# Performance work log

Measured on AMD Instinct MI355X. Metric: run time of the kernel, lower is better.

The kernel has to match this reference:

```python
import jax, jax.numpy as jnp
import numpy as np

PRECS = 1e-6
# [min, max] scaling ranges for the 12 XAJ parameters (order matches parameters[:, i, :])
PARA_SCALE = [[0.3, 2.0], [0.0, 5.0], [0.01, 100.0], [0.01, 100.0], [0.01, 200.0],
              [0.09, 1.0], [0.01, 100.0], [0.0, 10.0], [0.01, 0.7], [0.01, 0.7],
              [0.0, 0.998], [0.0, 0.998]]


def setup_inputs() -> dict:
    key = jax.random.key(0)
    k1, k2 = jax.random.split(key)
    Nstep, Ngrid, mu = 365, 2000, 8
    # col 0 = P (mm/d), col 2 = PET (mm/d); col 1 unused by the model
    x = jax.random.uniform(k1, (Nstep, Ngrid, 3), dtype=jnp.float32) * 10.0
    parameters = jax.random.uniform(k2, (Ngrid, 12, mu), dtype=jnp.float32)
    return {"x": x, "parameters": parameters, "mu": mu}


def _xaj(x, parameters, mu):
    P = x[:, :, 0]          # [T, Ngrid]
    PET = x[:, :, 2]        # [T, Ngrid]  (index 2, matching the original code)
    Ngrid = x.shape[1]

    sc = lambda a, i: PARA_SCALE[i][0] + a * (PARA_SCALE[i][1] - PARA_SCALE[i][0])
    (parKE, parB, parWUM, parWLM, parWM, parC, parSM, parEX,
     parKI_, parKG_, parCI, parCG) = [sc(parameters[:, i, :], i) for i in range(12)]

    wdm = jnp.maximum(parWM - parWUM - parWLM, 0.0)
    sum_k = parKI_ + parKG_
    parKI = jnp.where(sum_k < 1.0, parKI_, (1.0 - PRECS) * parKI_ / (sum_k + PRECS))
    parKG = jnp.where(sum_k < 1.0, parKG_, (1.0 - PRECS) * parKG_ / (sum_k + PRECS))

    init_state = jnp.full((Ngrid, mu), 0.001, dtype=jnp.float32)
    WU0 = WL0 = WD0 = S0 = QI0 = QG0 = FR0_init = init_state

    def step(carry, inp):
        WU, WL, WD, S, FR0, QI, QG = carry
        P_row, PET_row = inp                      # each [Ngrid]
        P_t = P_row[:, None]                      # broadcast over mu
        PET_t = PET_row[:, None] * parKE

        # three-layer evapotranspiration
        EU = jnp.minimum(PET_t, WU + P_t)
        D = jnp.maximum(PET_t - EU, 0.0)
        wet_excess = jnp.maximum(WL - parC * parWLM, 0.0)
        wet_ratio = wet_excess / (wet_excess + 1.0)
        EL_wet = D * WL / (parWLM + PRECS)
        EL_dry = jnp.minimum(parC * D, WL)
        EL = jnp.maximum(wet_ratio * EL_wet + (1.0 - wet_ratio) * EL_dry, 0.0)
        EL = jnp.minimum(EL, WL)
        D_res = jnp.maximum(D - EL, 0.0)
        ED = jnp.minimum(parC * D_res, WD)
        E = EU + EL + ED

        # saturation-excess runoff
        PE = jnp.maximum(P_t - E, 0.0)
        W = WU + WL + WD
        WMM = parWM * (1.0 + parB)
        base_W = jnp.maximum(1.0 - W / (parWM + PRECS), PRECS)
        A = WMM * (1.0 - base_W ** (1.0 / (1.0 + parB)))
        ratio = jnp.minimum((PE + A) / (WMM + PRECS), 1.0)
        R_per = jnp.where(PE + A < WMM,
                          PE - (parWM - W) + parWM * (1.0 - ratio) ** (1.0 + parB),
                          PE - (parWM - W))
        R_per = jnp.maximum(R_per, 0.0)

        # soil moisture update (fill top-down, deplete top-down)
        dW = P_t - E - R_per
        dpos = jnp.maximum(dW, 0.0)
        fill_u = jnp.minimum(dpos, jnp.maximum(parWUM - WU, 0.0))
        WU = WU + fill_u; dpos = dpos - fill_u
        fill_l = jnp.minimum(dpos, jnp.maximum(parWLM - WL, 0.0))
        WL = WL + fill_l; dpos = dpos - fill_l
        fill_d = jnp.minimum(dpos, jnp.maximum(wdm - WD, 0.0))
        WD = WD + fill_d
        dneg = jnp.maximum(-dW, 0.0)
        sub_u = jnp.minimum(dneg, WU)
        WU = WU - sub_u; dneg = dneg - sub_u
        sub_l = jnp.minimum(dneg, WL)
        WL = WL - sub_l; dneg = dneg - sub_l
        sub_d = jnp.minimum(dneg, WD)
        WD = WD - sub_d

        # free-water reservoir + three-flow separation
        FR_new = R_per / (PE + PRECS)
        FR = jnp.where(PE > 0.0, FR_new, FR0)
        FR = jnp.clip(FR, 0.0, 1.0)
        S_eq = jnp.minimum(S * FR0 / (FR + PRECS), parSM)
        SMM = parSM * (1.0 + parEX)
        ratio_s = jnp.maximum(1.0 - S_eq / (parSM + PRECS), PRECS)
        AU = SMM * (1.0 - ratio_s ** (1.0 / (1.0 + parEX)))
        ratio_pa = jnp.minimum((PE + AU) / (SMM + PRECS), 1.0)
        RS1 = (PE + S_eq - parSM + parSM * (1.0 - ratio_pa) ** (1.0 + parEX)) * FR
        RS2 = (PE + S_eq - parSM) * FR
        RS = jnp.where(PE + AU < SMM, RS1, RS2)
        RS = jnp.minimum(jnp.maximum(RS, 0.0), R_per)
        S = jnp.minimum(S_eq + (R_per - RS) / (FR + PRECS), parSM)
        RI = parKI * S * FR
        RG = parKG * S * FR
        S = S * (1.0 - parKI - parKG)

        # linear reservoirs
        QI = parCI * QI + (1.0 - parCI) * RI
        QG = parCG * QG + (1.0 - parCG) * RG

        return (WU, WL, WD, S, FR, QI, QG), (RS, QI, QG, E)

    carry0 = (WU0, WL0, WD0, S0, FR0_init, QI0, QG0)
    _, (QS_inflow, QI_inflow, QG_inflow, ET_series) = jax.lax.scan(step, carry0, (P, PET))

    QSave = QS_inflow.mean(-1, keepdims=True)
    QIave = QI_inflow.mean(-1, keepdims=True)
    QGave = QG_inflow.mean(-1, keepdims=True)
    ETave = ET_series.mean(-1, keepdims=True)
    river_inflow = QS_inflow + QI_inflow + QG_inflow
    Qs = river_inflow.mean(-1, keepdims=True)   # muwts is None
    # [Nstep, Ngrid, 5]
    return jnp.concatenate([Qs, QSave, QIave, QGave, ETave], axis=-1)


def reference(x, parameters, mu):
    return _xaj(x, parameters, mu)
```

## Files before the change

kernel.cpp:

```cpp
#include <hip/hip_runtime.h>

#define PRECS 1e-6f

__device__ __forceinline__ float fpow(float b, float e) {
    return __builtin_amdgcn_exp2f(e * __builtin_amdgcn_logf(b));
}

__device__ __forceinline__ float frcp(float v) {
    return __builtin_amdgcn_rcpf(v);
}

__device__ __forceinline__ float med3(float a, float b, float c) {
    return __builtin_amdgcn_fmed3f(a, b, c);
}

template <int CTRL>
__device__ __forceinline__ float dpp_mov(float v) {
    return __int_as_float(
        __builtin_amdgcn_update_dpp(0, __float_as_int(v), CTRL, 0xF, 0xF, true));
}

__device__ __forceinline__ float rsum8(float v) {
    v += dpp_mov<0xB1>(v);
    v += dpp_mov<0x4E>(v);
    v += dpp_mov<0x141>(v);
    return v;
}

__global__ __launch_bounds__(256, 1) void xaj_kernel(
    const float* __restrict__ x,
    const float* __restrict__ prm,
    float* __restrict__ out)
{
    constexpr int Nstep = 365, Ngrid = 2000;
    constexpr int xstride = Ngrid * 3;
    constexpr int K = 16;
    constexpr int NBLK = 23;
    constexpr int NPH  = NBLK + 3;

    const int wid  = (int)threadIdx.x >> 6;
    const int lane = (int)threadIdx.x & 63;
    const int g = blockIdx.x * 8 + (lane >> 3);
    const int m = lane & 7;

    __shared__ float2 stIn[2][K][64];
    __shared__ float4 stA[4][K][64];
    __shared__ float4 stFR[2][K][64];
    __shared__ float4 stB[2][K][64];

    const float lo[12] = {0.3f,0.0f,0.01f,0.01f,0.01f,0.09f,0.01f,0.0f,0.01f,0.01f,0.0f,0.0f};
    const float hi[12] = {2.0f,5.0f,100.0f,100.0f,200.0f,1.0f,100.0f,10.0f,0.7f,0.7f,0.998f,0.998f};
    float p[12];
    const float* pb = prm + (size_t)g * 96 + m;
#pragma unroll
    for (int i = 0; i < 12; ++i)
        p[i] = lo[i] + pb[i * 8] * (hi[i] - lo[i]);

    const float KE=p[0], B=p[1], WUM=p[2], WLM=p[3], WM=p[4], C=p[5],
                SM=p[6], EX=p[7], KI_=p[8], KG_=p[9], CI=p[10], CG=p[11];

    const float wdm  = fmaxf(WM - WUM - WLM, 0.f);
    const float sumk = KI_ + KG_;
    const float nrm  = (1.f - PRECS) / (sumk + PRECS);
    const float KI   = (sumk < 1.f) ? KI_ : KI_ * nrm;
    const float KG   = (sumk < 1.f) ? KG_ : KG_ * nrm;
    const float expB = 1.f + B,  invB  = 1.f / expB;
    const float WMM  = WM * expB;
    const float expEX= 1.f + EX, invEX = 1.f / expEX;
    const float SMM  = SM * expEX;
    const float inv_WLM = 1.f / (WLM + PRECS);
    const float inv_WM  = 1.f / (WM  + PRECS);
    const float inv_WMM = 1.f / (WMM + PRECS);
    const float inv_SM  = 1.f / (SM  + PRECS);
    const float inv_SMM = 1.f / (SMM + PRECS);
    const float oneK = 1.f - KI - KG;
    const float omCI = 1.f - CI, omCG = 1.f - CG;
    const float CWLM = C * WLM;
    const float inv1p = 1.f / (1.f + PRECS);
    const float eps2  = fmaxf(PRECS, fmaf(-SM, inv_SM, 1.f));
    const float powPRECS = fpow(PRECS, invB);

    float WU = 0.001f, WL = 0.001f, WD = 0.001f;
    float pw1;
    {
        const float W0 = 0.003f;
        pw1 = fpow(fmaxf(fmaf(-W0, inv_WM, 1.f), PRECS), invB);
    }
    float weC0   = fmaxf(WL - CWLM, 0.f);
    float wrC    = weC0 * frcp(1.f + weC0);
    float wlinvC = WL * inv_WLM;

    float Snc = 0.001f / oneK;
    float FRc = 0.001f, iFRc = frcp(0.001f + PRECS);
    float QI = 0.001f, QG = 0.001f;
    const float cKI = omCI * KI, cKG = omCG * KG;
    const float wa = (m == 0 || m == 1) ? 0.125f : 0.f;
    const float wb = (m == 0 || m == 2) ? 0.125f : 0.f;
    const float wc = (m == 0 || m == 3) ? 0.125f : 0.f;
    const float wd = (m >= 4) ? 0.125f : 0.f;
    const int   col = (m < 4) ? m : 4;
    float* outp = out + (size_t)g * 5 + col;
    const size_t ostr = (size_t)Ngrid * 5;
    const float* xg = x + (size_t)g * 3;
    float Pr[K], Er[K];

    auto ASTEP = [&](int ibuf, int obuf) {
        float2 rin[K];
#pragma unroll
        for (int k = 0; k < K; ++k)
            rin[k] = stIn[ibuf][k][lane];
#pragma unroll
        for (int k = 0; k < K; ++k) {
            const float Pt = rin[k].x, PET_t = rin[k].y;
            const float PETmP = PET_t - Pt;
            const float capD  = fmaxf(wdm, WD);
            const float M0 = fminf(PETmP, WU);
            const float D  = fmaxf(PETmP - WU, 0.f);
            const float ELwet = D * wlinvC;
            const float CD    = C * D;
            const float ELdry = fminf(CD, WL);
            const float EL    = med3(fmaf(wrC, ELwet - ELdry, ELdry), 0.f, WL);
            const float ED    = med3(fmaf(-C, EL, CD), 0.f, WD);
            const float SUME  = (M0 + EL) + ED;
            const float PE    = fmaxf(-SUME, 0.f);
            const float E     = Pt + SUME;
            const float W     = (WU + WL) + WD;
            const float omr   = fmaxf(fmaf(-PE, inv_WMM, pw1), 0.f);
            const float powr  = fpow(omr, expB);
            const float R_per = fmaxf(fmaf(WM, powr, PE + (W - WM)), 0.f);
            const float bwd  = fmaxf(fmaf(-(W - SUME), inv_WM, 1.f), PRECS);
            const float pw1d = fpow(bwd, invB);
            pw1 = (SUME < 0.f) ? fmaxf(omr, powPRECS) : pw1d;
            const float c0  = (WU - SUME) - R_per;
            const float WUn = med3(c0, 0.f, WUM);
            const float c1  = WL + (c0 - WUn);
            const float WLn = med3(c1, 0.f, WLM);
            const float c2  = WD + (c1 - WLn);
            const float WDn = med3(c2, 0.f, capD);
            WU = WUn; WL = WLn; WD = WDn;
            const float weN = fmaxf(WLn - CWLM, 0.f);
            wrC    = weN * frcp(1.f + weN);
            wlinvC = WLn * inv_WLM;
            stA[obuf][k][lane] = make_float4(PE, R_per, E, 0.f);
        }
    };

    auto BSTEP = [&](int abuf, int fbuf) {
        float4 ra[K], rg[K];
#pragma unroll
        for (int k = 0; k < K; ++k) ra[k] = stA[abuf][k][lane];
#pragma unroll
        for (int k = 0; k < K; ++k) rg[k] = stFR[fbuf][k][lane];
#pragma unroll
        for (int k = 0; k < K; ++k) {
            const float PE = ra[k].x, R_per = ra[k].y;
            const float FR = rg[k].x, iFR = rg[k].y;
            const float giFR = rg[k].z, r2 = rg[k].w;
            const float RpiFR = R_per * iFR;
            const float corr  = RpiFR - PE;
            const float S_eq    = fminf(Snc * giFR, SM);
            const float ratio_s = fmaxf(fmaf(-Snc, r2, 1.f), eps2);
            const float u   = fpow(ratio_s, invEX);
            const float om2 = fmaxf(fmaf(-PE, inv_SMM, u), 0.f);
            const float q   = fpow(om2, expEX);
            const float T   = fmaf(-SM, q, SM - S_eq);
            const float mq  = med3(T + corr, 0.f, RpiFR);
            const float Sn  = S_eq + mq;
            const float base = (PE - SM) + S_eq;
            const float RS = med3(fmaf(SM, q, base) * FR, 0.f, R_per);
            stB[fbuf][k][lane] = make_float4(RS, FR * Sn, ra[k].z, 0.f);
            Snc = Sn;
        }
    };

    auto CISSUE = [&](int blk) {
#pragma unroll
        for (int k = 0; k < K; ++k) {
            int t = blk * K + k;
            t = (t < Nstep) ? t : Nstep - 1;
            const float* xq = xg + (size_t)t * xstride;
            Pr[k] = xq[0];
            Er[k] = xq[2];
        }
    };
    auto CFR = [&](int abuf, int fbuf) {
#pragma unroll
        for (int k = 0; k < K; ++k) {
            const float4 ra = stA[abuf][k][lane];
            const float gk = oneK * FRc;
            const float q  = frcp(ra.x + PRECS);
            const float aa = ra.y * q;
            const float FRn  = fminf(aa, 1.f);
            const float iFRn = fmaxf(frcp(aa + PRECS), inv1p);
            const bool wet = ra.x > 0.f;
            FRc  = wet ? FRn  : FRc;
            iFRc = wet ? iFRn : iFRc;
            const float giFR = gk * iFRc;
            const float r2   = giFR * inv_SM;
            stFR[fbuf][k][lane] = make_float4(FRc, iFRc, giFR, r2);
        }
    };
    auto CWRITE = [&](int buf) {
#pragma unroll
        for (int k = 0; k < K; ++k)
            stIn[buf][k][lane] = make_float2(Pr[k], Er[k] * KE);
    };

    auto DSTEP = [&](int bbuf, int blk) {
        float4 rb[K];
#pragma unroll
        for (int k = 0; k < K; ++k) rb[k] = stB[bbuf][k][lane];
        const int t0 = blk * K;
#pragma unroll
        for (int k = 0; k < K; ++k) {
            QI = fmaf(CI, QI, cKI * rb[k].y);
            QG = fmaf(CG, QG, cKG * rb[k].y);
            const float u0 = rsum8(rb[k].x);
            const float u1 = rsum8(QI);
            const float u2 = rsum8(QG);
            const float u3 = rsum8(rb[k].z);
            const float v = fmaf(u0, wa, fmaf(u1, wb, fmaf(u2, wc, u3 * wd)));
            if (t0 + k < Nstep)
                outp[(size_t)(t0 + k) * ostr] = v;
        }
    };

    if (wid == 2) { CISSUE(0); CWRITE(0); }
    __syncthreads();

#pragma unroll 1
    for (int ph = 0; ph < NPH; ++ph) {
        if (wid == 0) {
            if (ph < NBLK) ASTEP(ph & 1, ph & 3);
        } else if (wid == 1) {
            if (ph >= 2 && ph < NBLK + 2) BSTEP((ph - 2) & 3, (ph - 2) & 1);
        } else if (wid == 2) {
            const bool ld = (ph + 1 < NBLK);
            if (ld) CISSUE(ph + 1);
            if (ph >= 1 && ph < NBLK + 1)
                CFR((ph - 1) & 3, (ph - 1) & 1);
            if (ld) CWRITE((ph + 1) & 1);
        } else {
            if (ph >= 3) DSTEP((ph - 3) & 1, ph - 3);
        }
        __syncthreads();
    }
}

extern "C" void kernel_launch(void* const* d_in, const int* in_sizes, int n_in,
                              void* d_out, int out_size, void* d_ws, size_t ws_size,
                              hipStream_t stream) {
    const float* x   = (const float*)d_in[0];
    const float* prm = (const float*)d_in[1];
    float* out = (float*)d_out;
    xaj_kernel<<<250, 256, 0, stream>>>(x, prm, out);
}
```

Before: 57.75 us.

## Replace lockstep block barriers with LDS flag-based producer-consumer pipeline between waves

The four specialized waves no longer advance in lockstep phases separated by __syncthreads. Each wave now runs its own loop and waits on per-stage LDS counters (acquire/release atomics with s_sleep polling). Input staging is deepened to four buffers so loads run two blocks ahead. Some work is also shifted: the A stage precomputes PE*inv_SMM, the FR stage precomputes R_per*iFR, the B stage uses a simplified med3 clamp for S, and stB shrinks to float2, with E read directly from stA. The aim is to let faster waves run ahead and remove barrier stalls, at the cost of spin-wait overhead and more complex buffer-reuse ordering.

After: 61.14 us. 1.06x slower.

```diff
diff --git a/kernel.cpp b/kernel.cpp
--- a/kernel.cpp
+++ b/kernel.cpp
@@ -25,6 +25,15 @@
     v += dpp_mov<0x4E>(v);
     v += dpp_mov<0x141>(v);
     return v;
+}
+
+__device__ __forceinline__ void waitge(int* f, int v) {
+    while (__hip_atomic_load(f, __ATOMIC_ACQUIRE, __HIP_MEMORY_SCOPE_WORKGROUP) < v)
+        __builtin_amdgcn_s_sleep(1);
+}
+__device__ __forceinline__ void setflag(int* f, int v) {
+    if ((threadIdx.x & 63) == 0)
+        __hip_atomic_store(f, v, __ATOMIC_RELEASE, __HIP_MEMORY_SCOPE_WORKGROUP);
 }
 
 __global__ __launch_bounds__(256, 1) void xaj_kernel(
@@ -36,17 +45,17 @@
     constexpr int xstride = Ngrid * 3;
     constexpr int K = 16;
     constexpr int NBLK = 23;
-    constexpr int NPH  = NBLK + 3;
 
     const int wid  = (int)threadIdx.x >> 6;
     const int lane = (int)threadIdx.x & 63;
     const int g = blockIdx.x * 8 + (lane >> 3);
     const int m = lane & 7;
 
-    __shared__ float2 stIn[2][K][64];
+    __shared__ float2 stIn[4][K][64];
     __shared__ float4 stA[4][K][64];
     __shared__ float4 stFR[2][K][64];
-    __shared__ float4 stB[2][K][64];
+    __shared__ float2 stB[2][K][64];
+    __shared__ int flg[8];
 
     const float lo[12] = {0.3f,0.0f,0.01f,0.01f,0.01f,0.09f,0.01f,0.0f,0.01f,0.01f,0.0f,0.0f};
     const float hi[12] = {2.0f,5.0f,100.0f,100.0f,200.0f,1.0f,100.0f,10.0f,0.7f,0.7f,0.998f,0.998f};
@@ -80,170 +89,184 @@
     const float eps2  = fmaxf(PRECS, fmaf(-SM, inv_SM, 1.f));
     const float powPRECS = fpow(PRECS, invB);
 
-    float WU = 0.001f, WL = 0.001f, WD = 0.001f;
-    float pw1;
-    {
-        const float W0 = 0.003f;
-        pw1 = fpow(fmaxf(fmaf(-W0, inv_WM, 1.f), PRECS), invB);
-    }
-    float weC0   = fmaxf(WL - CWLM, 0.f);
-    float wrC    = weC0 * frcp(1.f + weC0);
-    float wlinvC = WL * inv_WLM;
-
-    float Snc = 0.001f / oneK;
-    float FRc = 0.001f, iFRc = frcp(0.001f + PRECS);
-    float QI = 0.001f, QG = 0.001f;
-    const float cKI = omCI * KI, cKG = omCG * KG;
-    const float wa = (m == 0 || m == 1) ? 0.125f : 0.f;
-    const float wb = (m == 0 || m == 2) ? 0.125f : 0.f;
-    const float wc = (m == 0 || m == 3) ? 0.125f : 0.f;
-    const float wd = (m >= 4) ? 0.125f : 0.f;
-    const int   col = (m < 4) ? m : 4;
-    float* outp = out + (size_t)g * 5 + col;
-    const size_t ostr = (size_t)Ngrid * 5;
     const float* xg = x + (size_t)g * 3;
-    float Pr[K], Er[K];
-
-    auto ASTEP = [&](int ibuf, int obuf) {
-        float2 rin[K];
-#pragma unroll
-        for (int k = 0; k < K; ++k)
-            rin[k] = stIn[ibuf][k][lane];
-#pragma unroll
-        for (int k = 0; k < K; ++k) {
-            const float Pt = rin[k].x, PET_t = rin[k].y;
-            const float PETmP = PET_t - Pt;
-            const float capD  = fmaxf(wdm, WD);
-            const float M0 = fminf(PETmP, WU);
-            const float D  = fmaxf(PETmP - WU, 0.f);
-            const float ELwet = D * wlinvC;
-            const float CD    = C * D;
-            const float ELdry = fminf(CD, WL);
-            const float EL    = med3(fmaf(wrC, ELwet - ELdry, ELdry), 0.f, WL);
-            const float ED    = med3(fmaf(-C, EL, CD), 0.f, WD);
-            const float SUME  = (M0 + EL) + ED;
-            const float PE    = fmaxf(-SUME, 0.f);
-            const float E     = Pt + SUME;
-            const float W     = (WU + WL) + WD;
-            const float omr   = fmaxf(fmaf(-PE, inv_WMM, pw1), 0.f);
-            const float powr  = fpow(omr, expB);
-            const float R_per = fmaxf(fmaf(WM, powr, PE + (W - WM)), 0.f);
-            const float bwd  = fmaxf(fmaf(-(W - SUME), inv_WM, 1.f), PRECS);
-            const float pw1d = fpow(bwd, invB);
-            pw1 = (SUME < 0.f) ? fmaxf(omr, powPRECS) : pw1d;
-            const float c0  = (WU - SUME) - R_per;
-            const float WUn = med3(c0, 0.f, WUM);
-            const float c1  = WL + (c0 - WUn);
-            const float WLn = med3(c1, 0.f, WLM);
-            const float c2  = WD + (c1 - WLn);
-            const float WDn = med3(c2, 0.f, capD);
-            WU = WUn; WL = WLn; WD = WDn;
-            const float weN = fmaxf(WLn - CWLM, 0.f);
-            wrC    = weN * frcp(1.f + weN);
-            wlinvC = WLn * inv_WLM;
-            stA[obuf][k][lane] = make_float4(PE, R_per, E, 0.f);
-        }
-    };
-
-    auto BSTEP = [&](int abuf, int fbuf) {
-        float4 ra[K], rg[K];
-#pragma unroll
-        for (int k = 0; k < K; ++k) ra[k] = stA[abuf][k][lane];
-#pragma unroll
-        for (int k = 0; k < K; ++k) rg[k] = stFR[fbuf][k][lane];
-#pragma unroll
-        for (int k = 0; k < K; ++k) {
-            const float PE = ra[k].x, R_per = ra[k].y;
-            const float FR = rg[k].x, iFR = rg[k].y;
-            const float giFR = rg[k].z, r2 = rg[k].w;
-            const float RpiFR = R_per * iFR;
-            const float corr  = RpiFR - PE;
-            const float S_eq    = fminf(Snc * giFR, SM);
-            const float ratio_s = fmaxf(fmaf(-Snc, r2, 1.f), eps2);
-            const float u   = fpow(ratio_s, invEX);
-            const float om2 = fmaxf(fmaf(-PE, inv_SMM, u), 0.f);
-            const float q   = fpow(om2, expEX);
-            const float T   = fmaf(-SM, q, SM - S_eq);
-            const float mq  = med3(T + corr, 0.f, RpiFR);
-            const float Sn  = S_eq + mq;
-            const float base = (PE - SM) + S_eq;
-            const float RS = med3(fmaf(SM, q, base) * FR, 0.f, R_per);
-            stB[fbuf][k][lane] = make_float4(RS, FR * Sn, ra[k].z, 0.f);
-            Snc = Sn;
-        }
-    };
-
-    auto CISSUE = [&](int blk) {
-#pragma unroll
-        for (int k = 0; k < K; ++k) {
-            int t = blk * K + k;
-            t = (t < Nstep) ? t : Nstep - 1;
-            const float* xq = xg + (size_t)t * xstride;
-            Pr[k] = xq[0];
-            Er[k] = xq[2];
-        }
-    };
-    auto CFR = [&](int abuf, int fbuf) {
-#pragma unroll
-        for (int k = 0; k < K; ++k) {
-            const float4 ra = stA[abuf][k][lane];
-            const float gk = oneK * FRc;
-            const float q  = frcp(ra.x + PRECS);
-            const float aa = ra.y * q;
-            const float FRn  = fminf(aa, 1.f);
-            const float iFRn = fmaxf(frcp(aa + PRECS), inv1p);
-            const bool wet = ra.x > 0.f;
-            FRc  = wet ? FRn  : FRc;
-            iFRc = wet ? iFRn : iFRc;
-            const float giFR = gk * iFRc;
-            const float r2   = giFR * inv_SM;
-            stFR[fbuf][k][lane] = make_float4(FRc, iFRc, giFR, r2);
-        }
-    };
-    auto CWRITE = [&](int buf) {
-#pragma unroll
-        for (int k = 0; k < K; ++k)
-            stIn[buf][k][lane] = make_float2(Pr[k], Er[k] * KE);
-    };
-
-    auto DSTEP = [&](int bbuf, int blk) {
-        float4 rb[K];
-#pragma unroll
-        for (int k = 0; k < K; ++k) rb[k] = stB[bbuf][k][lane];
-        const int t0 = blk * K;
-#pragma unroll
-        for (int k = 0; k < K; ++k) {
-            QI = fmaf(CI, QI, cKI * rb[k].y);
-            QG = fmaf(CG, QG, cKG * rb[k].y);
-            const float u0 = rsum8(rb[k].x);
-            const float u1 = rsum8(QI);
-            const float u2 = rsum8(QG);
-            const float u3 = rsum8(rb[k].z);
-            const float v = fmaf(u0, wa, fmaf(u1, wb, fmaf(u2, wc, u3 * wd)));
-            if (t0 + k < Nstep)
-                outp[(size_t)(t0 + k) * ostr] = v;
-        }
-    };
-
-    if (wid == 2) { CISSUE(0); CWRITE(0); }
+
+    if (threadIdx.x < 8) flg[threadIdx.x] = 0;
     __syncthreads();
 
+    if (wid == 0) {
+        float WU = 0.001f, WL = 0.001f, WD = 0.001f;
+        float pw1;
+        {
+            const float W0 = 0.003f;
+            pw1 = fpow(fmaxf(fmaf(-W0, inv_WM, 1.f), PRECS), invB);
+        }
+        float weC0   = fmaxf(WL - CWLM, 0.f);
+        float wrC    = weC0 * frcp(1.f + weC0);
+        float wlinvC = WL * inv_WLM;
+
+        for (int pblk = 0; pblk < NBLK; ++pblk) {
+            waitge(&flg[0], pblk + 1);
+            waitge(&flg[3], pblk - 3);
+            waitge(&flg[2], pblk - 3);
+            waitge(&flg[4], pblk - 3);
+            float2 rin[K];
+#pragma unroll
+            for (int k = 0; k < K; ++k)
+                rin[k] = stIn[pblk & 3][k][lane];
+#pragma unroll
+            for (int k = 0; k < K; ++k) {
+                const float Pt = rin[k].x, PET_t = rin[k].y;
+                const float PETmP = PET_t - Pt;
+                const float capD  = fmaxf(wdm, WD);
+                const float M0 = fminf(PETmP, WU);
+                const float D  = fmaxf(PETmP - WU, 0.f);
+                const float ELwet = D * wlinvC;
+                const float CD    = C * D;
+                const float ELdry = fminf(CD, WL);
+                const float EL    = med3(fmaf(wrC, ELwet - ELdry, ELdry), 0.f, WL);
+                const float ED    = med3(fmaf(-C, EL, CD), 0.f, WD);
+                const float SUME  = (M0 + EL) + ED;
+                const float PE    = fmaxf(-SUME, 0.f);
+                const float E     = Pt + SUME;
+                const float W     = (WU + WL) + WD;
+                const float omr   = fmaxf(fmaf(-PE, inv_WMM, pw1), 0.f);
+                const float powr  = fpow(omr, expB);
+                const float R_per = fmaxf(fmaf(WM, powr, PE + (W - WM)), 0.f);
+                const float bwd  = fmaxf(fmaf(-(W - SUME), inv_WM, 1.f), PRECS);
+                const float pw1d = fpow(bwd, invB);
+                pw1 = (SUME < 0.f) ? fmaxf(omr, powPRECS) : pw1d;
+                const float c0  = (WU - SUME) - R_per;
+                const float WUn = med3(c0, 0.f, WUM);
+                const float c1  = WL + (c0 - WUn);
+                const float WLn = med3(c1, 0.f, WLM);
+                const float c2  = WD + (c1 - WLn);
+                const float WDn = med3(c2, 0.f, capD);
+                WU = WUn; WL = WLn; WD = WDn;
+                const float weN = fmaxf(WLn - CWLM, 0.f);
+                wrC    = weN * frcp(1.f + weN);
+                wlinvC = WLn * inv_WLM;
+                stA[pblk & 3][k][lane] =
+                    make_float4(PE, R_per, E, PE * inv_SMM);
+            }
+            setflag(&flg[1], pblk + 1);
+        }
+    } else if (wid == 1) {
+        float Snc = 0.001f / oneK;
+        for (int pblk = 0; pblk < NBLK; ++pblk) {
+            waitge(&flg[1], pblk + 1);
+            waitge(&flg[2], pblk + 1);
+            waitge(&flg[4], pblk - 1);
+            float4 ra[K], rf[K];
+#pragma unroll
+            for (int k = 0; k < K; ++k) ra[k] = stA[pblk & 3][k][lane];
+#pragma unroll
+            for (int k = 0; k < K; ++k) rf[k] = stFR[pblk & 1][k][lane];
+#pragma unroll
+            for (int k = 0; k < K; ++k) {
+                const float PE = ra[k].x, R_per = ra[k].y, PEc = ra[k].w;
+                const float FR = rf[k].x, r2 = rf[k].y;
+                const float giFR = rf[k].z, RpiFR = rf[k].w;
+                const float S_eq = fminf(Snc * giFR, SM);
+                const float ReS  = RpiFR + S_eq;
+                const float Kq   = (SM - PE) + RpiFR;
+                const float ratio_s = fmaxf(fmaf(-Snc, r2, 1.f), eps2);
+                const float u   = fpow(ratio_s, invEX);
+                const float om2 = fmaxf(u - PEc, 0.f);
+                const float q   = fpow(om2, expEX);
+                const float Sn  = med3(fmaf(-SM, q, Kq), S_eq, ReS);
+                const float RS = med3(fmaf(SM, q, (PE - SM) + S_eq) * FR,
+                                      0.f, R_per);
+                stB[pblk & 1][k][lane] = make_float2(RS, FR * Sn);
+                Snc = Sn;
+            }
+            setflag(&flg[3], pblk + 1);
+        }
+    } else if (wid == 2) {
+        float FRc = 0.001f, iFRc = frcp(0.001f + PRECS);
+        float Pr[K], Er[K];
 #pragma unroll 1
-    for (int ph = 0; ph < NPH; ++ph) {
-        if (wid == 0) {
-            if (ph < NBLK) ASTEP(ph & 1, ph & 3);
-        } else if (wid == 1) {
-            if (ph >= 2 && ph < NBLK + 2) BSTEP((ph - 2) & 3, (ph - 2) & 1);
-        } else if (wid == 2) {
-            const bool ld = (ph + 1 < NBLK);
-            if (ld) CISSUE(ph + 1);
-            if (ph >= 1 && ph < NBLK + 1)
-                CFR((ph - 1) & 3, (ph - 1) & 1);
-            if (ld) CWRITE((ph + 1) & 1);
-        } else {
-            if (ph >= 3) DSTEP((ph - 3) & 1, ph - 3);
-        }
-        __syncthreads();
+        for (int j = 0; j < 2; ++j) {
+#pragma unroll
+            for (int k = 0; k < K; ++k) {
+                const float* xq = xg + (size_t)(j * K + k) * xstride;
+                Pr[k] = xq[0]; Er[k] = xq[2];
+            }
+#pragma unroll
+            for (int k = 0; k < K; ++k)
+                stIn[j][k][lane] = make_float2(Pr[k], Er[k] * KE);
+            setflag(&flg[0], j + 1);
+        }
+        for (int j = 0; j < NBLK; ++j) {
+            const bool ld = (j + 2 < NBLK);
+            if (ld) {
+#pragma unroll
+                for (int k = 0; k < K; ++k) {
+                    int t = (j + 2) * K + k;
+                    t = (t < Nstep) ? t : Nstep - 1;
+                    const float* xq = xg + (size_t)t * xstride;
+                    Pr[k] = xq[0]; Er[k] = xq[2];
+                }
+            }
+            waitge(&flg[1], j + 1);
+            waitge(&flg[3], j - 1);
+#pragma unroll
+            for (int k = 0; k < K; ++k) {
+                const float4 ra = stA[j & 3][k][lane];
+                const float gk = oneK * FRc;
+                const float qq = frcp(ra.x + PRECS);
+                const float aa = ra.y * qq;
+                const float FRn  = fminf(aa, 1.f);
+                const float iFRn = fmaxf(frcp(aa + PRECS), inv1p);
+                const bool wet = ra.x > 0.f;
+                FRc  = wet ? FRn  : FRc;
+                iFRc = wet ? iFRn : iFRc;
+                const float giFR = gk * iFRc;
+                stFR[j & 1][k][lane] =
+                    make_float4(FRc, giFR * inv_SM, giFR, ra.y * iFRc);
+            }
+            setflag(&flg[2], j + 1);
+            if (ld) {
+#pragma unroll
+                for (int k = 0; k < K; ++k)
+                    stIn[(j + 2) & 3][k][lane] = make_float2(Pr[k], Er[k] * KE);
+                setflag(&flg[0], j + 3);
+            }
+        }
+    } else {
+        float QI = 0.001f, QG = 0.001f;
+        const float cKI = omCI * KI, cKG = omCG * KG;
+        const float wa = (m == 0 || m == 1) ? 0.125f : 0.f;
+        const float wb = (m == 0 || m == 2) ? 0.125f : 0.f;
+        const float wc = (m == 0 || m == 3) ? 0.125f : 0.f;
+        const float wd = (m >= 4) ? 0.125f : 0.f;
+        const int   col = (m < 4) ? m : 4;
+        float* outp = out + (size_t)g * 5 + col;
+        const size_t ostr = (size_t)Ngrid * 5;
+
+        for (int pblk = 0; pblk < NBLK; ++pblk) {
+            waitge(&flg[3], pblk + 1);
+            float2 rb[K];
+            float  re[K];
+#pragma unroll
+            for (int k = 0; k < K; ++k) rb[k] = stB[pblk & 1][k][lane];
+#pragma unroll
+            for (int k = 0; k < K; ++k) re[k] = stA[pblk & 3][k][lane].z;
+            const int t0 = pblk * K;
+#pragma unroll
+            for (int k = 0; k < K; ++k) {
+                QI = fmaf(CI, QI, cKI * rb[k].y);
+                QG = fmaf(CG, QG, cKG * rb[k].y);
+                const float u0 = rsum8(rb[k].x);
+                const float u1 = rsum8(QI);
+                const float u2 = rsum8(QG);
+                const float u3 = rsum8(re[k]);
+                const float v = fmaf(u0, wa, fmaf(u1, wb, fmaf(u2, wc, u3 * wd)));
+                if (t0 + k < Nstep)
+                    outp[(size_t)(t0 + k) * ostr] = v;
+            }
+            setflag(&flg[4], pblk + 1);
+        }
     }
 }
 
```
